# Performance work log

Measured on AMD Instinct MI355X. Metric: run time of the kernel, lower is better.

Reference implementation:

```python
import jax, jax.numpy as jnp
import numpy as np

NEG = -10000000000.0  # matches the torch module's additive mask value


def _span_attn(enc, logit_tok, starts, ends, qb, bsz):
    # enc: [bsz, seq, d]; logit_tok: [bsz, seq]; starts/ends/qb: [Q]
    seq = enc.shape[1]
    pos = jnp.arange(seq)
    # span mask: token t belongs to span iff start <= t <= end (inclusive)
    mask = (pos[None, :] >= starts[:, None]) & (pos[None, :] <= ends[:, None])  # [Q, seq]
    logits = logit_tok[qb] + (1.0 - mask.astype(enc.dtype)) * NEG               # [Q, seq]
    w = jax.nn.softmax(logits, axis=1)                                           # [Q, seq]
    # avoid materializing enc[qb] ([Q, seq, d]): contract against every batch row,
    # then select the right batch with a one-hot (p is tiny: [Q, bsz, d]).
    p = jnp.einsum('qs,bsd->qbd', w, enc)
    oh = jax.nn.one_hot(qb, bsz, dtype=enc.dtype)
    return jnp.einsum('qbd,qb->qd', p, oh)


def setup_inputs() -> dict:
    key = jax.random.key(0)
    ks = jax.random.split(key, 10)
    bsz, seq, hd, pd, Q = 8, 2048, 1024, 256, 8192
    enc = jax.random.normal(ks[0], (bsz, seq, hd), dtype=jnp.float32)
    proj_w = jax.random.normal(ks[1], (hd, pd), dtype=jnp.float32) * (1.0 / np.sqrt(hd))
    proj_b = jnp.zeros((pd,), dtype=jnp.float32)
    attn_w = jax.random.normal(ks[2], (pd,), dtype=jnp.float32) * (1.0 / np.sqrt(pd))
    attn_b = jnp.zeros((), dtype=jnp.float32)

    def make_spans(k):
        k1, k2, k3 = jax.random.split(k, 3)
        s = jax.random.randint(k1, (Q,), 0, seq)
        ln = jax.random.randint(k2, (Q,), 0, 32)
        e = jnp.minimum(s + ln, seq - 1)
        return s, e

    s1, e1 = make_spans(ks[3])
    s2, e2 = make_spans(ks[4])
    qb = jax.random.randint(ks[5], (Q,), 0, bsz)
    return {
        'flag': 0,
        'encoded_input': enc,
        'start_ids_1': s1,
        'end_ids_1': e1,
        'query_batch_idx': qb,
        'start_ids_2': s2,
        'end_ids_2': e2,
        'proj_w': proj_w,
        'proj_b': proj_b,
        'attn_w': attn_w,
        'attn_b': attn_b,
    }


def reference(flag, encoded_input, start_ids_1, end_ids_1, query_batch_idx,
              start_ids_2, end_ids_2, proj_w, proj_b, attn_w, attn_b):
    del flag  # unused in the original forward
    bsz = encoded_input.shape[0]
    enc = encoded_input @ proj_w + proj_b                 # use_proj=True path
    logit_tok = jnp.einsum('bsd,d->bs', enc, attn_w) + attn_b  # Linear(d,1)
    res1 = _span_attn(enc, logit_tok, start_ids_1, end_ids_1, query_batch_idx, bsz)
    res2 = _span_attn(enc, logit_tok, start_ids_2, end_ids_2, query_batch_idx, bsz)
    return (res1, res2)
```

## Files before the change

kernel.cpp:

```cpp
#include <hip/hip_runtime.h>

typedef __attribute__((ext_vector_type(8))) short bf16x8;
typedef __attribute__((ext_vector_type(4))) float f32x4;

#define LDK 40

__device__ __forceinline__ float bf2f(unsigned short u) {
    union { unsigned int i; float f; } v; v.i = ((unsigned int)u) << 16; return v.f;
}
__device__ __forceinline__ unsigned short f2bf(float f) {
    union { float f; unsigned int i; } v; v.f = f;
    unsigned int x = v.i;
    return (unsigned short)((x + 0x7FFFu + ((x >> 16) & 1u)) >> 16);
}

__global__ __launch_bounds__(256) void transpose_b_kernel(
    const float* __restrict__ B, unsigned short* __restrict__ Bt, int K, int N)
{
    __shared__ float tile[32][33];
    int kb = blockIdx.x % (K / 32);
    int nb = blockIdx.x / (K / 32);
    int k0 = kb * 32, n0 = nb * 32;
    int tx = threadIdx.x & 31, ty = threadIdx.x >> 5;
    #pragma unroll
    for (int i = 0; i < 4; ++i)
        tile[ty + 8 * i][tx] = B[(size_t)(k0 + ty + 8 * i) * N + n0 + tx];
    __syncthreads();
    #pragma unroll
    for (int i = 0; i < 4; ++i)
        Bt[(size_t)(n0 + ty + 8 * i) * K + k0 + tx] = f2bf(tile[tx][ty + 8 * i]);
}

__global__ __launch_bounds__(256) void gemm_mfma_kernel(
    const float* __restrict__ A, const unsigned short* __restrict__ Bt,
    const float* __restrict__ bias, unsigned short* __restrict__ C,
    int M, int N, int K)
{
    __shared__ unsigned short Asl[2][128 * LDK];
    __shared__ unsigned short Bsl[2][128 * LDK];

    const int tid = threadIdx.x;
    const int bid = blockIdx.x;
    const int xcd = bid & 7;
    const int j   = bid >> 3;
    const int bn  = (j & 1) * 128;
    const int bm  = (xcd * 16 + (j >> 1)) * 128;

    const int lane = tid & 63;
    const int wave = tid >> 6;
    const int wr = (wave >> 1) * 64;
    const int wc = (wave & 1) * 64;

    const int srow = tid >> 1;
    const int skh  = (tid & 1) * 16;
    const float*          Aptr = A  + (size_t)(bm + srow) * K + skh;
    const unsigned short* Bptr = Bt + (size_t)(bn + srow) * K + skh;

    float4 areg[4];
    uint4  breg[2];

    f32x4 acc[4][4];
    #pragma unroll
    for (int m = 0; m < 4; ++m)
        #pragma unroll
        for (int n = 0; n < 4; ++n)
            acc[m][n] = (f32x4){0.f, 0.f, 0.f, 0.f};

    const int c15 = lane & 15;
    const int kg8 = (lane >> 4) * 8;

    #define LOAD_TILE(k0)                                                     \
        {                                                                     \
            _Pragma("unroll")                                                 \
            for (int i = 0; i < 4; ++i)                                       \
                areg[i] = *(const float4*)(Aptr + (k0) + i * 4);              \
            const uint4* bp = (const uint4*)(Bptr + (k0));                    \
            breg[0] = bp[0];                                                  \
            breg[1] = bp[1];                                                  \
        }

    #define STORE_TILE(buf)                                                   \
        {                                                                     \
            unsigned short tmp[16];                                           \
            const float* af = (const float*)areg;                             \
            _Pragma("unroll")                                                 \
            for (int i = 0; i < 16; ++i) tmp[i] = f2bf(af[i]);                \
            *(bf16x8*)&Asl[buf][srow * LDK + skh]     = *(bf16x8*)&tmp[0];    \
            *(bf16x8*)&Asl[buf][srow * LDK + skh + 8] = *(bf16x8*)&tmp[8];    \
            *(uint4*)&Bsl[buf][srow * LDK + skh]      = breg[0];              \
            *(uint4*)&Bsl[buf][srow * LDK + skh + 8]  = breg[1];              \
        }

    const int nk = K / 32;

    LOAD_TILE(0)
    STORE_TILE(0)
    __syncthreads();

    for (int t = 0; t < nk; ++t) {
        if (t + 1 < nk) LOAD_TILE((t + 1) * 32)

        const int buf = t & 1;
        bf16x8 af[4], bfr[4];
        #pragma unroll
        for (int m = 0; m < 4; ++m)
            af[m] = *(bf16x8*)&Asl[buf][(wr + m * 16 + c15) * LDK + kg8];
        #pragma unroll
        for (int n = 0; n < 4; ++n)
            bfr[n] = *(bf16x8*)&Bsl[buf][(wc + n * 16 + c15) * LDK + kg8];
        #pragma unroll
        for (int m = 0; m < 4; ++m)
            #pragma unroll
            for (int n = 0; n < 4; ++n)
                acc[m][n] = __builtin_amdgcn_mfma_f32_16x16x32_bf16(
                    af[m], bfr[n], acc[m][n], 0, 0, 0);

        if (t + 1 < nk) {
            STORE_TILE((t + 1) & 1)
            __syncthreads();
        }
    }

    const int col0 = bn + wc + c15;
    const int row0 = bm + wr + (lane >> 4) * 4;
    #pragma unroll
    for (int n = 0; n < 4; ++n) {
        float bv = bias[col0 + n * 16];
        #pragma unroll
        for (int m = 0; m < 4; ++m) {
            #pragma unroll
            for (int i = 0; i < 4; ++i) {
                C[(size_t)(row0 + m * 16 + i) * N + col0 + n * 16] =
                    f2bf(acc[m][n][i] + bv);
            }
        }
    }
    #undef LOAD_TILE
    #undef STORE_TILE
}

__global__ __launch_bounds__(256) void logit_kernel(
    const unsigned short* __restrict__ enc, const float* __restrict__ attn_w,
    const float* __restrict__ attn_b, float* __restrict__ logit, int rows)
{
    int gid = blockIdx.x * 256 + threadIdx.x;
    int row = gid >> 6, lane = gid & 63;
    if (row >= rows) return;
    ushort4 ev = *(const ushort4*)(enc + (size_t)row * 256 + lane * 4);
    float4  w  = ((const float4*)attn_w)[lane];
    float s = bf2f(ev.x) * w.x + bf2f(ev.y) * w.y +
              bf2f(ev.z) * w.z + bf2f(ev.w) * w.w;
    #pragma unroll
    for (int off = 32; off; off >>= 1) s += __shfl_down(s, off, 64);
    if (lane == 0) logit[row] = s + attn_b[0];
}

__global__ __launch_bounds__(256) void span_kernel(
    const unsigned short* __restrict__ enc, const float* __restrict__ logit,
    const int* __restrict__ s1, const int* __restrict__ e1,
    const int* __restrict__ s2, const int* __restrict__ e2,
    const int* __restrict__ qb, float* __restrict__ out,
    int Q, int seq, int pd)
{
    int lane = threadIdx.x & 63;
    int q = blockIdx.x * 4 + (threadIdx.x >> 6);
    int r  = (q >= Q) ? 1 : 0;
    int qi = q - r * Q;
    int s = r ? s2[qi] : s1[qi];
    int e = r ? e2[qi] : e1[qi];
    int b = qb[qi];
    int len = e - s + 1;

    const float* lp = logit + (size_t)b * seq + s;
    float lg = (lane < len) ? lp[lane] : -3.4e38f;
    float m = lg;
    #pragma unroll
    for (int off = 32; off; off >>= 1) m = fmaxf(m, __shfl_xor(m, off, 64));
    float p = (lane < len) ? __expf(lg - m) : 0.0f;
    float sum = p;
    #pragma unroll
    for (int off = 32; off; off >>= 1) sum += __shfl_xor(sum, off, 64);
    float inv = 1.0f / sum;

    const unsigned short* ep = enc + ((size_t)b * seq + s) * pd + lane * 4;
    float ax = 0.f, ay = 0.f, az = 0.f, aw = 0.f;
    for (int t = 0; t < len; ++t) {
        float wt = __shfl(p, t, 64);
        ushort4 ev = *(const ushort4*)(ep + (size_t)t * pd);
        ax += wt * bf2f(ev.x);
        ay += wt * bf2f(ev.y);
        az += wt * bf2f(ev.z);
        aw += wt * bf2f(ev.w);
    }
    float4 res = {ax * inv, ay * inv, az * inv, aw * inv};
    *((float4*)(out + (size_t)q * pd) + lane) = res;
}

extern "C" void kernel_launch(void* const* d_in, const int* in_sizes, int n_in,
                              void* d_out, int out_size, void* d_ws, size_t ws_size,
                              hipStream_t stream) {
    const float* enc_in = (const float*)d_in[1];
    const int*   s1     = (const int*)d_in[2];
    const int*   e1     = (const int*)d_in[3];
    const int*   qb     = (const int*)d_in[4];
    const int*   s2     = (const int*)d_in[5];
    const int*   e2     = (const int*)d_in[6];
    const float* proj_w = (const float*)d_in[7];
    const float* proj_b = (const float*)d_in[8];
    const float* attn_w = (const float*)d_in[9];
    const float* attn_b = (const float*)d_in[10];
    float* out = (float*)d_out;

    const int Q   = in_sizes[2];
    const int pd  = in_sizes[8];
    const int hd  = in_sizes[7] / pd;
    const int seq = 2048;
    const int M   = in_sizes[1] / hd;

    unsigned short* enc_bf = (unsigned short*)d_ws;
    float*          logit  = (float*)((char*)d_ws + (size_t)M * pd * 2);
    unsigned short* Btw    = (unsigned short*)((char*)d_ws +
                               (size_t)M * pd * 2 + (size_t)M * 4);

    transpose_b_kernel<<<(hd / 32) * (pd / 32), 256, 0, stream>>>(proj_w, Btw, hd, pd);
    gemm_mfma_kernel<<<(M / 128) * (pd / 128), 256, 0, stream>>>(
        enc_in, Btw, proj_b, enc_bf, M, pd, hd);
    logit_kernel<<<M / 4, 256, 0, stream>>>(enc_bf, attn_w, attn_b, logit, M);
    span_kernel<<<2 * Q / 4, 256, 0, stream>>>(
        enc_bf, logit, s1, e1, s2, e2, qb, out, Q, seq, pd);
}
```

Before: 187.6 us.

## Shrink GEMM tiles to 64x64, unroll span loads by 8, drop attn_b

The projection GEMM moves from 128x128 to 64x64 block tiles with a 4-blocks-per-SM launch bound, producing 1024 blocks instead of 256 to fill more CUs. The span accumulation loop is unrolled by 8 so several row loads are in flight before the FMAs run. The attention bias add is removed from the logit kernel, since a constant shift cancels in softmax. Smaller tiles lower data reuse per block and raise global traffic for A and B.

```diff
diff --git a/kernel.cpp b/kernel.cpp
--- a/kernel.cpp
+++ b/kernel.cpp
@@ -31,39 +31,39 @@
         Bt[(size_t)(n0 + ty + 8 * i) * K + k0 + tx] = f2bf(tile[tx][ty + 8 * i]);
 }
 
-__global__ __launch_bounds__(256) void gemm_mfma_kernel(
+__global__ __launch_bounds__(256, 4) void gemm_mfma_kernel(
     const float* __restrict__ A, const unsigned short* __restrict__ Bt,
     const float* __restrict__ bias, unsigned short* __restrict__ C,
     int M, int N, int K)
 {
-    __shared__ unsigned short Asl[2][128 * LDK];
-    __shared__ unsigned short Bsl[2][128 * LDK];
+    __shared__ unsigned short Asl[2][64 * LDK];
+    __shared__ unsigned short Bsl[2][64 * LDK];
 
     const int tid = threadIdx.x;
     const int bid = blockIdx.x;
     const int xcd = bid & 7;
     const int j   = bid >> 3;
-    const int bn  = (j & 1) * 128;
-    const int bm  = (xcd * 16 + (j >> 1)) * 128;
+    const int bn  = (j & 3) * 64;
+    const int bm  = (xcd * 32 + (j >> 2)) * 64;
 
     const int lane = tid & 63;
     const int wave = tid >> 6;
-    const int wr = (wave >> 1) * 64;
-    const int wc = (wave & 1) * 64;
-
-    const int srow = tid >> 1;
-    const int skh  = (tid & 1) * 16;
-    const float*          Aptr = A  + (size_t)(bm + srow) * K + skh;
-    const unsigned short* Bptr = Bt + (size_t)(bn + srow) * K + skh;
-
-    float4 areg[4];
-    uint4  breg[2];
-
-    f32x4 acc[4][4];
-    #pragma unroll
-    for (int m = 0; m < 4; ++m)
-        #pragma unroll
-        for (int n = 0; n < 4; ++n)
+    const int wr = (wave >> 1) * 32;
+    const int wc = (wave & 1) * 32;
+
+    const int srow = tid >> 2;
+    const int sk   = (tid & 3) * 8;
+    const float*          Aptr = A  + (size_t)(bm + srow) * K + sk;
+    const unsigned short* Bptr = Bt + (size_t)(bn + srow) * K + sk;
+
+    float4 areg[2];
+    uint4  breg;
+
+    f32x4 acc[2][2];
+    #pragma unroll
+    for (int m = 0; m < 2; ++m)
+        #pragma unroll
+        for (int n = 0; n < 2; ++n)
             acc[m][n] = (f32x4){0.f, 0.f, 0.f, 0.f};
 
     const int c15 = lane & 15;
@@ -71,24 +71,19 @@
 
     #define LOAD_TILE(k0)                                                     \
         {                                                                     \
-            _Pragma("unroll")                                                 \
-            for (int i = 0; i < 4; ++i)                                       \
-                areg[i] = *(const float4*)(Aptr + (k0) + i * 4);              \
-            const uint4* bp = (const uint4*)(Bptr + (k0));                    \
-            breg[0] = bp[0];                                                  \
-            breg[1] = bp[1];                                                  \
+            areg[0] = *(const float4*)(Aptr + (k0));                          \
+            areg[1] = *(const float4*)(Aptr + (k0) + 4);                      \
+            breg    = *(const uint4*)(Bptr + (k0));                           \
         }
 
     #define STORE_TILE(buf)                                                   \
         {                                                                     \
-            unsigned short tmp[16];                                           \
+            unsigned short tmp[8];                                            \
             const float* af = (const float*)areg;                             \
             _Pragma("unroll")                                                 \
-            for (int i = 0; i < 16; ++i) tmp[i] = f2bf(af[i]);                \
-            *(bf16x8*)&Asl[buf][srow * LDK + skh]     = *(bf16x8*)&tmp[0];    \
-            *(bf16x8*)&Asl[buf][srow * LDK + skh + 8] = *(bf16x8*)&tmp[8];    \
-            *(uint4*)&Bsl[buf][srow * LDK + skh]      = breg[0];              \
-            *(uint4*)&Bsl[buf][srow * LDK + skh + 8]  = breg[1];              \
+            for (int i = 0; i < 8; ++i) tmp[i] = f2bf(af[i]);                 \
+            *(bf16x8*)&Asl[buf][srow * LDK + sk] = *(bf16x8*)&tmp[0];         \
+            *(uint4*)&Bsl[buf][srow * LDK + sk]  = breg;                      \
         }
 
     const int nk = K / 32;
@@ -101,17 +96,17 @@
         if (t + 1 < nk) LOAD_TILE((t + 1) * 32)
 
         const int buf = t & 1;
-        bf16x8 af[4], bfr[4];
-        #pragma unroll
-        for (int m = 0; m < 4; ++m)
+        bf16x8 af[2], bfr[2];
+        #pragma unroll
+        for (int m = 0; m < 2; ++m)
             af[m] = *(bf16x8*)&Asl[buf][(wr + m * 16 + c15) * LDK + kg8];
         #pragma unroll
-        for (int n = 0; n < 4; ++n)
+        for (int n = 0; n < 2; ++n)
             bfr[n] = *(bf16x8*)&Bsl[buf][(wc + n * 16 + c15) * LDK + kg8];
         #pragma unroll
-        for (int m = 0; m < 4; ++m)
+        for (int m = 0; m < 2; ++m)
             #pragma unroll
-            for (int n = 0; n < 4; ++n)
+            for (int n = 0; n < 2; ++n)
                 acc[m][n] = __builtin_amdgcn_mfma_f32_16x16x32_bf16(
                     af[m], bfr[n], acc[m][n], 0, 0, 0);
 
@@ -124,10 +119,10 @@
     const int col0 = bn + wc + c15;
     const int row0 = bm + wr + (lane >> 4) * 4;
     #pragma unroll
-    for (int n = 0; n < 4; ++n) {
+    for (int n = 0; n < 2; ++n) {
         float bv = bias[col0 + n * 16];
         #pragma unroll
-        for (int m = 0; m < 4; ++m) {
+        for (int m = 0; m < 2; ++m) {
             #pragma unroll
             for (int i = 0; i < 4; ++i) {
                 C[(size_t)(row0 + m * 16 + i) * N + col0 + n * 16] =
@@ -141,7 +136,7 @@
 
 __global__ __launch_bounds__(256) void logit_kernel(
     const unsigned short* __restrict__ enc, const float* __restrict__ attn_w,
-    const float* __restrict__ attn_b, float* __restrict__ logit, int rows)
+    float* __restrict__ logit, int rows)
 {
     int gid = blockIdx.x * 256 + threadIdx.x;
     int row = gid >> 6, lane = gid & 63;
@@ -152,7 +147,7 @@
               bf2f(ev.z) * w.z + bf2f(ev.w) * w.w;
     #pragma unroll
     for (int off = 32; off; off >>= 1) s += __shfl_down(s, off, 64);
-    if (lane == 0) logit[row] = s + attn_b[0];
+    if (lane == 0) logit[row] = s;
 }
 
 __global__ __launch_bounds__(256) void span_kernel(
@@ -184,7 +179,23 @@
 
     const unsigned short* ep = enc + ((size_t)b * seq + s) * pd + lane * 4;
     float ax = 0.f, ay = 0.f, az = 0.f, aw = 0.f;
-    for (int t = 0; t < len; ++t) {
+
+    int t = 0;
+    for (; t + 8 <= len; t += 8) {
+        ushort4 ev[8];
+        #pragma unroll
+        for (int u = 0; u < 8; ++u)
+            ev[u] = *(const ushort4*)(ep + (size_t)(t + u) * pd);
+        #pragma unroll
+        for (int u = 0; u < 8; ++u) {
+            float wt = __shfl(p, t + u, 64);
+            ax += wt * bf2f(ev[u].x);
+            ay += wt * bf2f(ev[u].y);
+            az += wt * bf2f(ev[u].z);
+            aw += wt * bf2f(ev[u].w);
+        }
+    }
+    for (; t < len; ++t) {
         float wt = __shfl(p, t, 64);
         ushort4 ev = *(const ushort4*)(ep + (size_t)t * pd);
         ax += wt * bf2f(ev.x);
@@ -208,7 +219,6 @@
     const float* proj_w = (const float*)d_in[7];
     const float* proj_b = (const float*)d_in[8];
     const float* attn_w = (const float*)d_in[9];
-    const float* attn_b = (const float*)d_in[10];
     float* out = (float*)d_out;
 
     const int Q   = in_sizes[2];
@@ -223,9 +233,9 @@
                                (size_t)M * pd * 2 + (size_t)M * 4);
 
     transpose_b_kernel<<<(hd / 32) * (pd / 32), 256, 0, stream>>>(proj_w, Btw, hd, pd);
-    gemm_mfma_kernel<<<(M / 128) * (pd / 128), 256, 0, stream>>>(
+    gemm_mfma_kernel<<<(M / 64) * (pd / 64), 256, 0, stream>>>(
         enc_in, Btw, proj_b, enc_bf, M, pd, hd);
-    logit_kernel<<<M / 4, 256, 0, stream>>>(enc_bf, attn_w, attn_b, logit, M);
+    logit_kernel<<<M / 4, 256, 0, stream>>>(enc_bf, attn_w, logit, M);
     span_kernel<<<2 * Q / 4, 256, 0, stream>>>(
         enc_bf, logit, s1, e1, s2, e2, qb, out, Q, seq, pd);
 }
```

Result: faster. 170.3 us (-9.2%).
